# Performance work log

Measured on AMD Instinct MI355X. Metric: run time of the kernel, lower is better.

## Reference

```python
import math
import jax, jax.numpy as jnp
import numpy as np

N = 1024          # num_gaussians
W = 256           # image width
H = 256           # image height
C = 1             # grayscale -> 1 channel
BD = 2.0          # init bound
EPS2D = 0.3       # gsplat low-pass filter on 2D covariance


def setup_inputs() -> dict:
    key = jax.random.key(0)
    ks = jax.random.split(key, 8)
    # grid-initialized means (matches _init_gaussians for 2dgs)
    grid_size = int(math.ceil(math.sqrt(N)))
    lin = jnp.linspace(-BD, BD, grid_size)
    gx, gy = jnp.meshgrid(lin, lin, indexing='xy')
    grid_xy = jnp.stack([gx.ravel(), gy.ravel()], axis=1)[:N]
    noise = (jax.random.uniform(ks[0], (N, 2)) - 0.5) * (2 * BD / grid_size) * 0.5
    means = jnp.concatenate([grid_xy + noise, jnp.zeros((N, 1))], axis=1)      # [N,3]
    scales = jnp.concatenate([jax.random.uniform(ks[1], (N, 2)) * 0.5 + 0.1,
                              jnp.full((N, 1), 0.01)], axis=1)                  # [N,3]
    quats = jax.random.uniform(ks[2], (N,)) * (2.0 * math.pi)                   # [N] in-plane angle
    rgbs = jax.scipy.special.logit(jax.random.uniform(ks[3], (N, C)) * 0.3 + 0.1)
    opacities = jax.scipy.special.logit(jax.random.uniform(ks[4], (N,)) * 0.5 + 0.1)
    fov_x = math.pi / 2.0
    focal = 0.5 * W / math.tan(0.5 * fov_x)
    viewmat = jnp.array([[1.0, 0.0, 0.0, 0.0],
                         [0.0, 1.0, 0.0, 0.0],
                         [0.0, 0.0, 1.0, 8.0],
                         [0.0, 0.0, 0.0, 1.0]], dtype=jnp.float32)
    K = jnp.array([[focal, 0.0, W / 2.0],
                   [0.0, focal, H / 2.0],
                   [0.0, 0.0, 1.0]], dtype=jnp.float32)
    return {"means": means, "quats": quats, "scales": scales, "rgbs": rgbs,
            "opacities": opacities, "viewmat": viewmat, "K": K}


def _render(means, quats, scales, rgbs, opacities, viewmat, K):
    Rv, t = viewmat[:3, :3], viewmat[:3, 3]
    p_cam = means @ Rv.T + t                                # [N,3] camera-space
    x, y, z = p_cam[:, 0], p_cam[:, 1], p_cam[:, 2]
    fx, fy, cx, cy = K[0, 0], K[1, 1], K[0, 2], K[1, 2]
    inv_z = 1.0 / z
    u = fx * x * inv_z + cx                                 # [N] pixel means
    v = fy * y * inv_z + cy

    # 3D covariance: rotation about z-axis by angle theta (2DGS disk)
    ct, st = jnp.cos(quats), jnp.sin(quats)
    zr, on = jnp.zeros_like(ct), jnp.ones_like(ct)
    R3 = jnp.stack([jnp.stack([ct, -st, zr], -1),
                    jnp.stack([st,  ct, zr], -1),
                    jnp.stack([zr,  zr, on], -1)], -2)      # [N,3,3]
    M = R3 * scales[:, None, :]                             # R @ diag(s)
    cov3 = M @ jnp.swapaxes(M, -1, -2)                      # [N,3,3]
    cov_cam = jnp.einsum('ij,njk,lk->nil', Rv, cov3, Rv)    # [N,3,3]

    # perspective projection Jacobian -> 2D covariance
    j0 = jnp.stack([fx * inv_z, zr, -fx * x * inv_z * inv_z], -1)
    j1 = jnp.stack([zr, fy * inv_z, -fy * y * inv_z * inv_z], -1)
    J = jnp.stack([j0, j1], -2)                             # [N,2,3]
    cov2 = jnp.einsum('nij,njk,nlk->nil', J, cov_cam, J)    # [N,2,2]
    a = cov2[:, 0, 0] + EPS2D
    b = cov2[:, 0, 1]
    c = cov2[:, 1, 1] + EPS2D
    det = a * c - b * b
    conic_a, conic_b, conic_c = c / det, -b / det, a / det  # inverse covariance

    op = jax.nn.sigmoid(opacities)                          # torch.sigmoid(self.opacities)
    colors = jax.nn.sigmoid(rgbs)                           # torch.sigmoid(self.rgbs)

    # global front-to-back depth sort
    order = jnp.argsort(z)
    u, v = u[order], v[order]
    ca, cb, cc = conic_a[order], conic_b[order], conic_c[order]
    op, colors = op[order], colors[order]

    # pixel centers
    px = jnp.arange(W, dtype=jnp.float32) + 0.5
    py = jnp.arange(H, dtype=jnp.float32) + 0.5
    gx, gy = jnp.meshgrid(px, py)                           # [H,W]
    dx = gx.ravel()[:, None] - u[None, :]                   # [P,N]
    dy = gy.ravel()[:, None] - v[None, :]
    sigma = 0.5 * (ca * dx * dx + cc * dy * dy) + cb * dx * dy
    alpha = jnp.clip(op * jnp.exp(-jnp.maximum(sigma, 0.0)), 0.0, 0.999)

    # alpha compositing: T_i = prod_{j<i} (1 - alpha_j)
    logT = jnp.cumsum(jnp.log1p(-alpha), axis=1)
    P = H * W
    T = jnp.exp(jnp.concatenate([jnp.zeros((P, 1), alpha.dtype), logT[:, :-1]], axis=1))
    weights = alpha * T                                     # [P,N]
    img = weights @ colors                                  # [P,C]
    return img.reshape(H, W, C).transpose(2, 0, 1)[None]    # [1,C,H,W]


def reference(means, quats, scales, rgbs, opacities, viewmat, K):
    return _render(means, quats, scales, rgbs, opacities, viewmat, K)
```

## Files before the change

### kernel.cpp

```cpp
#include <hip/hip_runtime.h>

#define NG     1024
#define IMG_W  256
#define IMG_H  256
#define NWAVE  16
#define LOG2E  1.44269504088896340736f
#define INV2PI 0.15915494309189533577f
#define CULL_E (-16.0f)
#define PXC    128.0f

#define CAP0 512
#define CAP1 832
#define CAP2 832
#define CAP3 512
#define OFF0 0
#define OFF1 512
#define OFF2 1344
#define OFF3 2176
#define LTOT 2688

__global__ __launch_bounds__(1024, 1) void gs_fused(
    const float* __restrict__ means, const float* __restrict__ quats,
    const float* __restrict__ scales, const float* __restrict__ rgbs,
    const float* __restrict__ opacities, const float* __restrict__ viewmat,
    const float* __restrict__ Kmat, float* __restrict__ out)
{
    __shared__ float4 sL[LTOT];
    __shared__ float  pcb[2][NWAVE][64];
    __shared__ float  pTb[2][NWAVE][64];
    __shared__ int    sCnt[4][NWAVE];

    const int tid  = threadIdx.x;
    const int wave = tid >> 6;
    const int lane = tid & 63;
    const int b    = blockIdx.x;
    const int r0 = (b + 64)  & 255;
    const int r1 = b;
    const int r2 = (b + 128) & 255;
    const int r3 = (b + 192) & 255;

    float R00=viewmat[0], R01=viewmat[1], R02=viewmat[2],  t0=viewmat[3];
    float R10=viewmat[4], R11=viewmat[5], R12=viewmat[6],  t1=viewmat[7];
    float R20=viewmat[8], R21=viewmat[9], R22=viewmat[10], t2=viewmat[11];
    float fx=Kmat[0], cx=Kmat[2], fy=Kmat[4], cy=Kmat[5];
    float m0=means[3*tid+0], m1=means[3*tid+1], m2=means[3*tid+2];
    float xc = R00*m0 + R01*m1 + R02*m2 + t0;
    float yc = R10*m0 + R11*m1 + R12*m2 + t1;
    float zc = R20*m0 + R21*m1 + R22*m2 + t2;
    float iz = __builtin_amdgcn_rcpf(zc);
    float u  = fx*xc*iz + cx;
    float v  = fy*yc*iz + cy;
    float j00 = fx*iz, j02 = -fx*xc*iz*iz;
    float j11 = fy*iz, j12 = -fy*yc*iz*iz;
    float P00 = j00*R00 + j02*R20;
    float P01 = j00*R01 + j02*R21;
    float P02 = j00*R02 + j02*R22;
    float P10 = j11*R10 + j12*R20;
    float P11 = j11*R11 + j12*R21;
    float P12 = j11*R12 + j12*R22;
    float qr = quats[tid] * INV2PI;
    float ct = __builtin_amdgcn_cosf(qr);
    float st = __builtin_amdgcn_sinf(qr);
    float s0=scales[3*tid+0], s1=scales[3*tid+1], s2=scales[3*tid+2];
    float Q00 = (P00*ct + P01*st) * s0;
    float Q01 = (P01*ct - P00*st) * s1;
    float Q02 = P02 * s2;
    float Q10 = (P10*ct + P11*st) * s0;
    float Q11 = (P11*ct - P10*st) * s1;
    float Q12 = P12 * s2;
    float a  = Q00*Q00 + Q01*Q01 + Q02*Q02 + 0.3f;
    float bb = Q00*Q10 + Q01*Q11 + Q02*Q12;
    float c  = Q10*Q10 + Q11*Q11 + Q12*Q12 + 0.3f;
    float idet = __builtin_amdgcn_rcpf(a*c - bb*bb);
    float tex  = __builtin_amdgcn_exp2f(-opacities[tid]*LOG2E);
    float l2op = -__builtin_amdgcn_logf(1.0f + tex);
    float cex  = __builtin_amdgcn_exp2f(-rgbs[tid]*LOG2E);
    float col  = __builtin_amdgcn_rcpf(1.0f + cex);
    float Ax = -0.5f*LOG2E*c*idet;
    float Bb =  LOG2E*bb*idet;
    float Cy = -0.5f*LOG2E*a*idet;
    float Hv = bb * __builtin_amdgcn_rcpf(c);
    float ut = u - PXC;

    float Bp0, Cp0, Bp1, Cp1, Bp2, Cp2, Bp3, Cp3;
    int   k0, k1, k2, k3;
#define FOLD(J, RJ, BPJ, CPJ, KEEPJ) do {                                   \
        float dy = ((float)(RJ) + 0.5f) - v;                                \
        float C1 = __builtin_fmaf(Cy, dy*dy, l2op);                         \
        float Bd = Bb * dy;                                                 \
        BPJ = __builtin_fmaf(-(Ax+Ax), ut, Bd);                             \
        float tq = __builtin_fmaf(Ax, ut, -Bd);                             \
        CPJ = __builtin_fmaf(tq, ut, C1);                                   \
        float pxv = __builtin_fmaf(Hv, dy, ut);                             \
        float lo = (float)((J)*64) + 0.5f - PXC;                            \
        float pq = __builtin_fminf(__builtin_fmaxf(pxv, lo), lo + 63.0f);   \
        float em = __builtin_fmaf(__builtin_fmaf(Ax, pq, BPJ), pq, CPJ);    \
        KEEPJ = (em > CULL_E) ? 1 : 0;                                      \
    } while (0)
    FOLD(0, r0, Bp0, Cp0, k0);
    FOLD(1, r1, Bp1, Cp1, k1);
    FOLD(2, r2, Bp2, Cp2, k2);
    FOLD(3, r3, Bp3, Cp3, k3);
#undef FOLD

    unsigned long long bal0 = __ballot(k0);
    unsigned long long bal1 = __ballot(k1);
    unsigned long long bal2 = __ballot(k2);
    unsigned long long bal3 = __ballot(k3);
    if (lane == 0) {
        sCnt[0][wave] = __popcll(bal0);
        sCnt[1][wave] = __popcll(bal1);
        sCnt[2][wave] = __popcll(bal2);
        sCnt[3][wave] = __popcll(bal3);
    }
    __syncthreads();
    int base0=0, base1=0, base2=0, base3=0;
    int M0=0, M1=0, M2=0, M3=0;
    #pragma unroll
    for (int w = 0; w < NWAVE; ++w) {
        int c0=sCnt[0][w], c1=sCnt[1][w], c2=sCnt[2][w], c3=sCnt[3][w];
        if (w < wave) { base0+=c0; base1+=c1; base2+=c2; base3+=c3; }
        M0+=c0; M1+=c1; M2+=c2; M3+=c3;
    }
    unsigned long long below = (1ULL << lane) - 1ULL;
    {
        int o0 = base0 + __popcll(bal0 & below);
        int o1 = base1 + __popcll(bal1 & below);
        int o2 = base2 + __popcll(bal2 & below);
        int o3 = base3 + __popcll(bal3 & below);
        if (k0 && o0 < CAP0) sL[OFF0 + o0] = make_float4(Ax, Bp0, Cp0, col);
        if (k1 && o1 < CAP1) sL[OFF1 + o1] = make_float4(Ax, Bp1, Cp1, col);
        if (k2 && o2 < CAP2) sL[OFF2 + o2] = make_float4(Ax, Bp2, Cp2, col);
        if (k3 && o3 < CAP3) sL[OFF3 + o3] = make_float4(Ax, Bp3, Cp3, col);
    }
    __syncthreads();

    int Ms0 = M0 < CAP0 ? M0 : CAP0;
    int Ms1 = M1 < CAP1 ? M1 : CAP1;
    int Ms2 = M2 < CAP2 ? M2 : CAP2;
    int Ms3 = M3 < CAP3 ? M3 : CAP3;

#define COMPOSITE(J, OFFJ, MSJ, BUF) do {                                   \
        int seg = (MSJ + NWAVE - 1) >> 4;                                   \
        int n0  = wave * seg;                                               \
        int n1  = n0 + seg; if (n1 > MSJ) n1 = MSJ;                         \
        float p  = (float)((J)*64 + lane) + 0.5f - PXC;                     \
        float Tc = 1.0f, cc = 0.0f;                                         \
        for (int ch = n0; ch < n1; ch += 8) {                               \
            int ce = ch + 8; if (ce > n1) ce = n1;                          \
            _Pragma("unroll 8")                                             \
            for (int n = ch; n < ce; ++n) {                                 \
                float4 G = sL[OFFJ + n];                                    \
                float e  = __builtin_fmaf(__builtin_fmaf(G.x, p, G.y), p, G.z); \
                float al = __builtin_amdgcn_exp2f(e);                       \
                float w  = al * Tc;                                         \
                cc = __builtin_fmaf(w, G.w, cc);                            \
                Tc -= w;                                                    \
            }                                                               \
            if (__all(Tc < 1e-6f)) break;                                   \
        }                                                                   \
        pcb[BUF][wave][lane] = cc;                                          \
        pTb[BUF][wave][lane] = Tc;                                          \
    } while (0)
#define MERGE(BUF, RJ, J) do {                                              \
        float ca = pcb[BUF][0][lane];                                       \
        float Ta = pTb[BUF][0][lane];                                       \
        _Pragma("unroll")                                                   \
        for (int w = 1; w < NWAVE; ++w) {                                   \
            ca = __builtin_fmaf(Ta, pcb[BUF][w][lane], ca);                 \
            Ta *= pTb[BUF][w][lane];                                        \
        }                                                                   \
        out[(RJ) * IMG_W + (J)*64 + lane] = ca;                             \
    } while (0)

    COMPOSITE(0, OFF0, Ms0, 0);
    __syncthreads();
    COMPOSITE(1, OFF1, Ms1, 1);
    if (wave == 15) MERGE(0, r0, 0);
    __syncthreads();
    COMPOSITE(2, OFF2, Ms2, 0);
    if (wave == 14) MERGE(1, r1, 1);
    __syncthreads();
    COMPOSITE(3, OFF3, Ms3, 1);
    if (wave == 13) MERGE(0, r2, 2);
    __syncthreads();
    if (wave == 12) MERGE(1, r3, 3);
#undef COMPOSITE
#undef MERGE
}

extern "C" void kernel_launch(void* const* d_in, const int* in_sizes, int n_in,
                              void* d_out, int out_size, void* d_ws, size_t ws_size,
                              hipStream_t stream) {
    const float* means     = (const float*)d_in[0];
    const float* quats     = (const float*)d_in[1];
    const float* scales    = (const float*)d_in[2];
    const float* rgbs      = (const float*)d_in[3];
    const float* opacities = (const float*)d_in[4];
    const float* viewmat   = (const float*)d_in[5];
    const float* Kmat      = (const float*)d_in[6];
    float* out = (float*)d_out;

    gs_fused<<<IMG_H, 1024, 0, stream>>>(means, quats, scales, rgbs,
                                         opacities, viewmat, Kmat, out);
}
```

Measured before the change: 13.55 us.

## Run all four column composites before one barrier and drop early-exit check

Each wave now composites all four column segments back to back into separate per-segment partial buffers, so only one barrier is needed before the merges, which are split across four waves. The per-chunk wave-wide transmittance early-exit test is removed and the inner loop is unrolled by four. This cuts three block barriers and the vote overhead, at the cost of doubling the partial-result shared memory and always walking the full segment even when transmittance is exhausted.

```diff
diff --git a/kernel.cpp b/kernel.cpp
--- a/kernel.cpp
+++ b/kernel.cpp
@@ -26,8 +26,8 @@
     const float* __restrict__ Kmat, float* __restrict__ out)
 {
     __shared__ float4 sL[LTOT];
-    __shared__ float  pcb[2][NWAVE][64];
-    __shared__ float  pTb[2][NWAVE][64];
+    __shared__ float  pcb[4][NWAVE][64];
+    __shared__ float  pTb[4][NWAVE][64];
     __shared__ int    sCnt[4][NWAVE];
 
     const int tid  = threadIdx.x;
@@ -140,51 +140,46 @@
     int Ms2 = M2 < CAP2 ? M2 : CAP2;
     int Ms3 = M3 < CAP3 ? M3 : CAP3;
 
-#define COMPOSITE(J, OFFJ, MSJ, BUF) do {                                   \
+#define COMPOSITE(J, OFFJ, MSJ) do {                                        \
         int seg = (MSJ + NWAVE - 1) >> 4;                                   \
         int n0  = wave * seg;                                               \
         int n1  = n0 + seg; if (n1 > MSJ) n1 = MSJ;                         \
         float p  = (float)((J)*64 + lane) + 0.5f - PXC;                     \
         float Tc = 1.0f, cc = 0.0f;                                         \
-        for (int ch = n0; ch < n1; ch += 8) {                               \
-            int ce = ch + 8; if (ce > n1) ce = n1;                          \
-            _Pragma("unroll 8")                                             \
-            for (int n = ch; n < ce; ++n) {                                 \
-                float4 G = sL[OFFJ + n];                                    \
-                float e  = __builtin_fmaf(__builtin_fmaf(G.x, p, G.y), p, G.z); \
-                float al = __builtin_amdgcn_exp2f(e);                       \
-                float w  = al * Tc;                                         \
-                cc = __builtin_fmaf(w, G.w, cc);                            \
-                Tc -= w;                                                    \
-            }                                                               \
-            if (__all(Tc < 1e-6f)) break;                                   \
+        _Pragma("unroll 4")                                                 \
+        for (int n = n0; n < n1; ++n) {                                     \
+            float4 G = sL[OFFJ + n];                                        \
+            float e  = __builtin_fmaf(__builtin_fmaf(G.x, p, G.y), p, G.z); \
+            float al = __builtin_amdgcn_exp2f(e);                           \
+            float w  = al * Tc;                                             \
+            cc = __builtin_fmaf(w, G.w, cc);                                \
+            Tc -= w;                                                        \
         }                                                                   \
-        pcb[BUF][wave][lane] = cc;                                          \
-        pTb[BUF][wave][lane] = Tc;                                          \
+        pcb[J][wave][lane] = cc;                                            \
+        pTb[J][wave][lane] = Tc;                                            \
     } while (0)
-#define MERGE(BUF, RJ, J) do {                                              \
-        float ca = pcb[BUF][0][lane];                                       \
-        float Ta = pTb[BUF][0][lane];                                       \
+
+    COMPOSITE(0, OFF0, Ms0);
+    COMPOSITE(1, OFF1, Ms1);
+    COMPOSITE(2, OFF2, Ms2);
+    COMPOSITE(3, OFF3, Ms3);
+    __syncthreads();
+
+#define MERGE(J, RJ) do {                                                   \
+        float ca = pcb[J][0][lane];                                         \
+        float Ta = pTb[J][0][lane];                                         \
         _Pragma("unroll")                                                   \
         for (int w = 1; w < NWAVE; ++w) {                                   \
-            ca = __builtin_fmaf(Ta, pcb[BUF][w][lane], ca);                 \
-            Ta *= pTb[BUF][w][lane];                                        \
+            ca = __builtin_fmaf(Ta, pcb[J][w][lane], ca);                   \
+            Ta *= pTb[J][w][lane];                                          \
         }                                                                   \
         out[(RJ) * IMG_W + (J)*64 + lane] = ca;                             \
     } while (0)
 
-    COMPOSITE(0, OFF0, Ms0, 0);
-    __syncthreads();
-    COMPOSITE(1, OFF1, Ms1, 1);
-    if (wave == 15) MERGE(0, r0, 0);
-    __syncthreads();
-    COMPOSITE(2, OFF2, Ms2, 0);
-    if (wave == 14) MERGE(1, r1, 1);
-    __syncthreads();
-    COMPOSITE(3, OFF3, Ms3, 1);
-    if (wave == 13) MERGE(0, r2, 2);
-    __syncthreads();
-    if (wave == 12) MERGE(1, r3, 3);
+    if      (wave == 15) MERGE(0, r0);
+    else if (wave == 14) MERGE(1, r1);
+    else if (wave == 13) MERGE(2, r2);
+    else if (wave == 12) MERGE(3, r3);
 #undef COMPOSITE
 #undef MERGE
 }
```

Result: faster. 12.15 us (-10.3%).
